# Optimization experiments

Measured on AMD Instinct MI355X. Metric: run time of the kernel, lower is better.

The kernel has to match this reference:

```python
import jax, jax.numpy as jnp
import numpy as np

IN_SIZE = 64
RES = 1024
B = 16
T = 2048
ALPHA = 0.5
SPECTRAL_RADIUS = 0.9


def setup_inputs() -> dict:
    key = jax.random.key(0)
    ks = jax.random.split(key, 8)
    # W_hh scaled so spectral radius ~ SPECTRAL_RADIUS (circular law: |eig|max ~ sqrt(R)*std)
    scale_hh = SPECTRAL_RADIUS / np.sqrt(RES)
    return {
        "x": jax.random.normal(ks[0], (B, T, IN_SIZE), dtype=jnp.float32),
        "W_in0": jax.random.normal(ks[1], (IN_SIZE, RES), dtype=jnp.float32) * 0.5,
        "W_hh0": jax.random.normal(ks[2], (RES, RES), dtype=jnp.float32) * scale_hh,
        "b0": jax.random.normal(ks[3], (1, RES), dtype=jnp.float32) * 0.5,
        "W_in1": jax.random.normal(ks[4], (RES, RES), dtype=jnp.float32) * 0.1,
        "W_hh1": jax.random.normal(ks[5], (RES, RES), dtype=jnp.float32) * scale_hh,
        "b1": jax.random.normal(ks[6], (1, RES), dtype=jnp.float32) * 0.5,
        "readout": jax.random.normal(ks[7], (2 * RES, IN_SIZE), dtype=jnp.float32) * 0.02,
    }


def _reservoir_layer(xs, W_in, W_hh, b, alpha):
    # xs: [T, B, F] time-major; sequential leaky-integrator scan over T
    h0 = jnp.zeros((xs.shape[1], W_hh.shape[0]), dtype=xs.dtype)

    def step(h, x_i):
        h = (1.0 - alpha) * h + alpha * jnp.tanh(x_i @ W_in + h @ W_hh + b)
        return h, h

    _, states = jax.lax.scan(step, h0, xs)
    return states  # [T, B, R]


def reference(x, W_in0, W_hh0, b0, W_in1, W_hh1, b1, readout):
    xt = jnp.transpose(x, (1, 0, 2))  # [T, B, in]
    s0 = _reservoir_layer(xt, W_in0, W_hh0, b0, ALPHA)  # [T, B, R]
    s1 = _reservoir_layer(s0, W_in1, W_hh1, b1, ALPHA)  # [T, B, R]
    h = jnp.concatenate([s0, s1], axis=-1)  # [T, B, 2R]
    out = h @ readout  # [T, B, in]
    return jnp.transpose(out, (1, 0, 2))  # [B, T, in]
```

## Files before the change

kernel.cpp:

```cpp
#include <hip/hip_runtime.h>
#include <math.h>

#define ESN_B 16
#define ESN_T 2048
#define ESN_R 1024
#define ESN_IN 64
#define NBR (ESN_B * ESN_R)

#define OFF_WT_HH0 0
#define OFF_WT_IN1 (1024 * 1024)
#define OFF_WT_HH1 (2 * 1024 * 1024)
#define OFF_WT_IN0 (3 * 1024 * 1024)
#define OFF_RT     (OFF_WT_IN0 + 1024 * 64)
#define OFF_S0G    (OFF_RT + 64 * 2048)
#define OFF_S1G    (OFF_S0G + 2 * NBR)
#define OFF_FLAGS  (OFF_S1G + 2 * NBR)

__global__ void __launch_bounds__(256) transpose_k(const float* __restrict__ src,
                                                   float* __restrict__ dst,
                                                   int rows, int cols) {
  __shared__ float tile[32][33];
  int bx = blockIdx.x * 32, by = blockIdx.y * 32;
  int tx = threadIdx.x, ty = threadIdx.y;
  #pragma unroll
  for (int i = ty; i < 32; i += 8) {
    int r = by + i, c = bx + tx;
    if (r < rows && c < cols) tile[i][tx] = src[(size_t)r * cols + c];
  }
  __syncthreads();
  #pragma unroll
  for (int i = ty; i < 32; i += 8) {
    int c = bx + i, r = by + tx;
    if (c < cols && r < rows) dst[(size_t)c * rows + r] = tile[tx][i];
  }
}

__device__ __forceinline__ float fast_tanh(float v) {
  float a = fabsf(v);
  float e = __expf(-2.0f * a);
  float t = __fdividef(1.0f - e, 1.0f + e);
  return copysignf(t, v);
}

__device__ __forceinline__ float dot4(float4 a, float4 b, float acc) {
  acc = fmaf(a.x, b.x, acc);
  acc = fmaf(a.y, b.y, acc);
  acc = fmaf(a.z, b.z, acc);
  acc = fmaf(a.w, b.w, acc);
  return acc;
}

__device__ __forceinline__ float wave_red64(float v) {
  #pragma unroll
  for (int off = 32; off > 0; off >>= 1) v += __shfl_xor(v, off, 64);
  return v;
}

__device__ __forceinline__ float reduce4(float a0, float a1, float a2, float a3,
                                         bool lb0, bool lb1) {
  float uA = lb0 ? a0 : a1, kA = lb0 ? a1 : a0;
  float A = kA + __shfl_xor(uA, 1, 64);
  float uB = lb0 ? a2 : a3, kB = lb0 ? a3 : a2;
  float B = kB + __shfl_xor(uB, 1, 64);
  float uC = lb1 ? A : B, kC = lb1 ? B : A;
  float C = kC + __shfl_xor(uC, 2, 64);
  C += __shfl_xor(C, 4, 64);
  C += __shfl_xor(C, 8, 64);
  C += __shfl_xor(C, 16, 64);
  C += __shfl_xor(C, 32, 64);
  return C;
}

__device__ __forceinline__ void llc_store_f32(float* p, float v) {
  asm volatile("global_store_dword %0, %1, off sc1" :: "v"(p), "v"(v) : "memory");
}
__device__ __forceinline__ void llc_store_u32(unsigned* p, unsigned v) {
  asm volatile("global_store_dword %0, %1, off sc1" :: "v"(p), "v"(v) : "memory");
}
__device__ __forceinline__ void vmcnt0() {
  asm volatile("s_waitcnt vmcnt(0)" ::: "memory");
}

__global__ void __launch_bounds__(256, 1) esn_scan_kernel(
    const float* __restrict__ x,
    const float* __restrict__ b0,
    const float* __restrict__ b1,
    float* __restrict__ wsf,
    float* __restrict__ out) {
  __shared__ float s0l[2][4][1024];
  __shared__ float s1l[4][1024];

  const float* wtHH0 = wsf + OFF_WT_HH0;
  const float* wtIN1 = wsf + OFF_WT_IN1;
  const float* wtHH1 = wsf + OFF_WT_HH1;
  const float* wtIN0 = wsf + OFF_WT_IN0;
  const float* rt    = wsf + OFF_RT;
  float* s0g = wsf + OFF_S0G;
  float* s1g = wsf + OFF_S1G;
  unsigned* flags = (unsigned*)(wsf + OFF_FLAGS);

  const int tid = threadIdx.x;
  const int l = tid & 63;
  const int w = tid >> 6;
  const int bid = blockIdx.x;
  const int g = bid >> 6;
  const int bg = bid & 63;
  const int batch0 = g * 4;
  const int c0 = (bg * 4 + w) * 4;
  const int wg = bg * 4 + w;
  const int rbl = wg >> 6;
  const int rb = batch0 + rbl;
  const int roc = wg & 63;
  unsigned* gflags = flags + g * 64;
  const bool lb0 = (l & 1) != 0;
  const bool lb1 = (l & 2) != 0;

  float4 whh0[4][4], win1[4][4], whh1[4][4], rdt[8];
  float win0v[4];
  #pragma unroll
  for (int cc = 0; cc < 4; ++cc) {
    const float* p0 = wtHH0 + (size_t)(c0 + cc) * ESN_R + l * 4;
    const float* p1 = wtIN1 + (size_t)(c0 + cc) * ESN_R + l * 4;
    const float* p2 = wtHH1 + (size_t)(c0 + cc) * ESN_R + l * 4;
    #pragma unroll
    for (int q = 0; q < 4; ++q) {
      whh0[cc][q] = *(const float4*)(p0 + q * 256);
      win1[cc][q] = *(const float4*)(p1 + q * 256);
      whh1[cc][q] = *(const float4*)(p2 + q * 256);
    }
    win0v[cc] = wtIN0[(size_t)(c0 + cc) * ESN_IN + l];
  }
  #pragma unroll
  for (int q = 0; q < 8; ++q)
    rdt[q] = *(const float4*)(rt + (size_t)roc * 2048 + q * 256 + l * 4);
  const float b0sel = b0[c0 + (l & 3)];
  const float b1sel = b1[c0 + (l & 3)];

  for (int r = 0; r < ESN_T + 2; ++r) {
    const int slot = r & 1, oslot = slot ^ 1;
    const bool doL0 = (r < ESN_T);
    const bool doL1 = (r >= 1 && r <= ESN_T);

    float xv[4];
    if (doL0) {
      #pragma unroll
      for (int bb = 0; bb < 4; ++bb)
        xv[bb] = x[((size_t)(batch0 + bb) * ESN_T + r) * ESN_IN + l];
    }

    if (r > 0) {
      if (w == 0) {
        const unsigned* fp = &gflags[l];
        unsigned f;
        do {
          asm volatile("global_load_dword %0, %1, off sc1\n\ts_waitcnt vmcnt(0)"
                       : "=v"(f) : "v"(fp) : "memory");
        } while (!__all(f >= (unsigned)r));
      }
      __syncthreads();
    }

    {
      const float* gs0 = s0g + oslot * NBR + batch0 * ESN_R + tid * 4;
      const float* gs1 = s1g + oslot * NBR + batch0 * ESN_R + tid * 4;
      float4 t0, t1, t2, t3, u0, u1, u2, u3;
      asm volatile(
          "global_load_dwordx4 %0, %8, off sc1\n\t"
          "global_load_dwordx4 %1, %9, off sc1\n\t"
          "global_load_dwordx4 %2, %10, off sc1\n\t"
          "global_load_dwordx4 %3, %11, off sc1\n\t"
          "global_load_dwordx4 %4, %12, off sc1\n\t"
          "global_load_dwordx4 %5, %13, off sc1\n\t"
          "global_load_dwordx4 %6, %14, off sc1\n\t"
          "global_load_dwordx4 %7, %15, off sc1\n\t"
          "s_waitcnt vmcnt(0)"
          : "=&v"(t0), "=&v"(t1), "=&v"(t2), "=&v"(t3),
            "=&v"(u0), "=&v"(u1), "=&v"(u2), "=&v"(u3)
          : "v"(gs0), "v"(gs0 + 1024), "v"(gs0 + 2048), "v"(gs0 + 3072),
            "v"(gs1), "v"(gs1 + 1024), "v"(gs1 + 2048), "v"(gs1 + 3072)
          : "memory");
      float* d0 = &s0l[slot][0][0] + tid * 4;
      float* d1 = &s1l[0][0] + tid * 4;
      *(float4*)(d0)        = t0;
      *(float4*)(d0 + 1024) = t1;
      *(float4*)(d0 + 2048) = t2;
      *(float4*)(d0 + 3072) = t3;
      *(float4*)(d1)        = u0;
      *(float4*)(d1 + 1024) = u1;
      *(float4*)(d1 + 2048) = u2;
      *(float4*)(d1 + 3072) = u3;
    }
    __syncthreads();

    for (int bb = 0; bb < 4; ++bb) {
      float4 h0f[4];
      #pragma unroll
      for (int q = 0; q < 4; ++q)
        h0f[q] = *(const float4*)(&s0l[slot][bb][q * 256 + l * 4]);

      if (doL0) {
        float a0 = xv[bb] * win0v[0], a1 = xv[bb] * win0v[1];
        float a2 = xv[bb] * win0v[2], a3 = xv[bb] * win0v[3];
        #pragma unroll
        for (int q = 0; q < 4; ++q) {
          a0 = dot4(whh0[0][q], h0f[q], a0);
          a1 = dot4(whh0[1][q], h0f[q], a1);
          a2 = dot4(whh0[2][q], h0f[q], a2);
          a3 = dot4(whh0[3][q], h0f[q], a3);
        }
        float C = reduce4(a0, a1, a2, a3, lb0, lb1);
        if (l < 4) {
          float prev = s0l[slot][bb][c0 + l];
          float nv = 0.5f * prev + 0.5f * fast_tanh(C + b0sel);
          llc_store_f32(&s0g[slot * NBR + (batch0 + bb) * ESN_R + c0 + l], nv);
        }
      }
      if (doL1) {
        float4 h1f[4];
        #pragma unroll
        for (int q = 0; q < 4; ++q)
          h1f[q] = *(const float4*)(&s1l[bb][q * 256 + l * 4]);
        float a0 = 0.f, a1 = 0.f, a2 = 0.f, a3 = 0.f;
        #pragma unroll
        for (int q = 0; q < 4; ++q) {
          a0 = dot4(win1[0][q], h0f[q], a0); a0 = dot4(whh1[0][q], h1f[q], a0);
          a1 = dot4(win1[1][q], h0f[q], a1); a1 = dot4(whh1[1][q], h1f[q], a1);
          a2 = dot4(win1[2][q], h0f[q], a2); a2 = dot4(whh1[2][q], h1f[q], a2);
          a3 = dot4(win1[3][q], h0f[q], a3); a3 = dot4(whh1[3][q], h1f[q], a3);
        }
        float C = reduce4(a0, a1, a2, a3, lb0, lb1);
        if (l < 4) {
          float prev = s1l[bb][c0 + l];
          float nv = 0.5f * prev + 0.5f * fast_tanh(C + b1sel);
          llc_store_f32(&s1g[slot * NBR + (batch0 + bb) * ESN_R + c0 + l], nv);
        }
      }
    }

    vmcnt0();
    __syncthreads();
    if (tid == 0) llc_store_u32(&gflags[bg], (unsigned)(r + 1));

    if (r >= 2) {
      float a = 0.f;
      #pragma unroll
      for (int q = 0; q < 4; ++q)
        a = dot4(rdt[q], *(const float4*)(&s0l[oslot][rbl][q * 256 + l * 4]), a);
      #pragma unroll
      for (int q = 0; q < 4; ++q)
        a = dot4(rdt[q + 4], *(const float4*)(&s1l[rbl][q * 256 + l * 4]), a);
      a = wave_red64(a);
      if (l == 0) out[((size_t)rb * ESN_T + (r - 2)) * ESN_IN + roc] = a;
    }
  }
}

extern "C" void kernel_launch(void* const* d_in, const int* in_sizes, int n_in,
                              void* d_out, int out_size, void* d_ws, size_t ws_size,
                              hipStream_t stream) {
  (void)in_sizes; (void)n_in; (void)out_size; (void)ws_size;
  const float* x     = (const float*)d_in[0];
  const float* w_in0 = (const float*)d_in[1];
  const float* w_hh0 = (const float*)d_in[2];
  const float* b0    = (const float*)d_in[3];
  const float* w_in1 = (const float*)d_in[4];
  const float* w_hh1 = (const float*)d_in[5];
  const float* b1    = (const float*)d_in[6];
  const float* rdo   = (const float*)d_in[7];
  float* out = (float*)d_out;
  float* wsf = (float*)d_ws;

  dim3 tb(32, 8);
  transpose_k<<<dim3(32, 32), tb, 0, stream>>>(w_hh0, wsf + OFF_WT_HH0, 1024, 1024);
  transpose_k<<<dim3(32, 32), tb, 0, stream>>>(w_in1, wsf + OFF_WT_IN1, 1024, 1024);
  transpose_k<<<dim3(32, 32), tb, 0, stream>>>(w_hh1, wsf + OFF_WT_HH1, 1024, 1024);
  transpose_k<<<dim3(32, 2),  tb, 0, stream>>>(w_in0, wsf + OFF_WT_IN0, 64, 1024);
  transpose_k<<<dim3(2, 64),  tb, 0, stream>>>(rdo,   wsf + OFF_RT, 2048, 64);

  hipMemsetAsync(wsf + OFF_S0G + NBR, 0, NBR * sizeof(float), stream);
  hipMemsetAsync(wsf + OFF_S1G, 0, NBR * sizeof(float), stream);
  hipMemsetAsync(wsf + OFF_FLAGS, 0, 4 * 64 * sizeof(unsigned), stream);

  esn_scan_kernel<<<dim3(256), dim3(256), 0, stream>>>(x, b0, b1, wsf, out);
}
```

Baseline: 13.83 ms.

## Split grid-wide step barrier into separate layer-0 and layer-1 flag phases

Replaces the single per-step cross-block flag barrier with two flag arrays, one per reservoir layer. Layer-0 state is staged, computed and published, and its flag is raised before layer-1 work begins. Layer 1 then waits on its own flag before staging and computing. The intent is to shorten the layer-0 recurrence critical path so other blocks can start the next step sooner. The cost is an extra global polling phase and more block-level synchronisation per timestep.

```diff
diff --git a/kernel.cpp b/kernel.cpp
--- a/kernel.cpp
+++ b/kernel.cpp
@@ -77,8 +77,33 @@
 __device__ __forceinline__ void llc_store_u32(unsigned* p, unsigned v) {
   asm volatile("global_store_dword %0, %1, off sc1" :: "v"(p), "v"(v) : "memory");
 }
+__device__ __forceinline__ unsigned llc_load_u32(const unsigned* p) {
+  unsigned f;
+  asm volatile("global_load_dword %0, %1, off sc1\n\ts_waitcnt vmcnt(0)"
+               : "=v"(f) : "v"(p) : "memory");
+  return f;
+}
 __device__ __forceinline__ void vmcnt0() {
   asm volatile("s_waitcnt vmcnt(0)" ::: "memory");
+}
+
+__device__ __forceinline__ void stage4k(const float* gsrc, float* ldst, int tid) {
+  float4 t0, t1, t2, t3;
+  const float* p = gsrc + tid * 4;
+  asm volatile(
+      "global_load_dwordx4 %0, %4, off sc1\n\t"
+      "global_load_dwordx4 %1, %5, off sc1\n\t"
+      "global_load_dwordx4 %2, %6, off sc1\n\t"
+      "global_load_dwordx4 %3, %7, off sc1\n\t"
+      "s_waitcnt vmcnt(0)"
+      : "=&v"(t0), "=&v"(t1), "=&v"(t2), "=&v"(t3)
+      : "v"(p), "v"(p + 1024), "v"(p + 2048), "v"(p + 3072)
+      : "memory");
+  float* d = ldst + tid * 4;
+  *(float4*)(d)        = t0;
+  *(float4*)(d + 1024) = t1;
+  *(float4*)(d + 2048) = t2;
+  *(float4*)(d + 3072) = t3;
 }
 
 __global__ void __launch_bounds__(256, 1) esn_scan_kernel(
@@ -111,7 +136,8 @@
   const int rbl = wg >> 6;
   const int rb = batch0 + rbl;
   const int roc = wg & 63;
-  unsigned* gflags = flags + g * 64;
+  unsigned* gflag0 = flags + g * 64;
+  unsigned* gflag1 = flags + 256 + g * 64;
   const bool lb0 = (l & 1) != 0;
   const bool lb1 = (l & 2) != 0;
 
@@ -150,55 +176,20 @@
 
     if (r > 0) {
       if (w == 0) {
-        const unsigned* fp = &gflags[l];
-        unsigned f;
-        do {
-          asm volatile("global_load_dword %0, %1, off sc1\n\ts_waitcnt vmcnt(0)"
-                       : "=v"(f) : "v"(fp) : "memory");
-        } while (!__all(f >= (unsigned)r));
+        while (!__all(llc_load_u32(&gflag0[l]) >= (unsigned)r)) {}
       }
       __syncthreads();
     }
 
-    {
-      const float* gs0 = s0g + oslot * NBR + batch0 * ESN_R + tid * 4;
-      const float* gs1 = s1g + oslot * NBR + batch0 * ESN_R + tid * 4;
-      float4 t0, t1, t2, t3, u0, u1, u2, u3;
-      asm volatile(
-          "global_load_dwordx4 %0, %8, off sc1\n\t"
-          "global_load_dwordx4 %1, %9, off sc1\n\t"
-          "global_load_dwordx4 %2, %10, off sc1\n\t"
-          "global_load_dwordx4 %3, %11, off sc1\n\t"
-          "global_load_dwordx4 %4, %12, off sc1\n\t"
-          "global_load_dwordx4 %5, %13, off sc1\n\t"
-          "global_load_dwordx4 %6, %14, off sc1\n\t"
-          "global_load_dwordx4 %7, %15, off sc1\n\t"
-          "s_waitcnt vmcnt(0)"
-          : "=&v"(t0), "=&v"(t1), "=&v"(t2), "=&v"(t3),
-            "=&v"(u0), "=&v"(u1), "=&v"(u2), "=&v"(u3)
-          : "v"(gs0), "v"(gs0 + 1024), "v"(gs0 + 2048), "v"(gs0 + 3072),
-            "v"(gs1), "v"(gs1 + 1024), "v"(gs1 + 2048), "v"(gs1 + 3072)
-          : "memory");
-      float* d0 = &s0l[slot][0][0] + tid * 4;
-      float* d1 = &s1l[0][0] + tid * 4;
-      *(float4*)(d0)        = t0;
-      *(float4*)(d0 + 1024) = t1;
-      *(float4*)(d0 + 2048) = t2;
-      *(float4*)(d0 + 3072) = t3;
-      *(float4*)(d1)        = u0;
-      *(float4*)(d1 + 1024) = u1;
-      *(float4*)(d1 + 2048) = u2;
-      *(float4*)(d1 + 3072) = u3;
-    }
-    __syncthreads();
-
-    for (int bb = 0; bb < 4; ++bb) {
-      float4 h0f[4];
-      #pragma unroll
-      for (int q = 0; q < 4; ++q)
-        h0f[q] = *(const float4*)(&s0l[slot][bb][q * 256 + l * 4]);
-
-      if (doL0) {
+    stage4k(s0g + oslot * NBR + batch0 * ESN_R, &s0l[slot][0][0], tid);
+    __syncthreads();
+
+    if (doL0) {
+      for (int bb = 0; bb < 4; ++bb) {
+        float4 h0f[4];
+        #pragma unroll
+        for (int q = 0; q < 4; ++q)
+          h0f[q] = *(const float4*)(&s0l[slot][bb][q * 256 + l * 4]);
         float a0 = xv[bb] * win0v[0], a1 = xv[bb] * win0v[1];
         float a2 = xv[bb] * win0v[2], a3 = xv[bb] * win0v[3];
         #pragma unroll
@@ -215,11 +206,29 @@
           llc_store_f32(&s0g[slot * NBR + (batch0 + bb) * ESN_R + c0 + l], nv);
         }
       }
-      if (doL1) {
-        float4 h1f[4];
-        #pragma unroll
-        for (int q = 0; q < 4; ++q)
+    }
+    vmcnt0();
+    __syncthreads();
+    if (tid == 0) llc_store_u32(&gflag0[bg], (unsigned)(r + 1));
+
+    if (r > 1) {
+      if (w == 0) {
+        while (!__all(llc_load_u32(&gflag1[l]) >= (unsigned)r)) {}
+      }
+    }
+    __syncthreads();
+
+    stage4k(s1g + oslot * NBR + batch0 * ESN_R, &s1l[0][0], tid);
+    __syncthreads();
+
+    if (doL1) {
+      for (int bb = 0; bb < 4; ++bb) {
+        float4 h0f[4], h1f[4];
+        #pragma unroll
+        for (int q = 0; q < 4; ++q) {
+          h0f[q] = *(const float4*)(&s0l[slot][bb][q * 256 + l * 4]);
           h1f[q] = *(const float4*)(&s1l[bb][q * 256 + l * 4]);
+        }
         float a0 = 0.f, a1 = 0.f, a2 = 0.f, a3 = 0.f;
         #pragma unroll
         for (int q = 0; q < 4; ++q) {
@@ -236,10 +245,9 @@
         }
       }
     }
-
     vmcnt0();
     __syncthreads();
-    if (tid == 0) llc_store_u32(&gflags[bg], (unsigned)(r + 1));
+    if (tid == 0) llc_store_u32(&gflag1[bg], (unsigned)(r + 1));
 
     if (r >= 2) {
       float a = 0.f;
@@ -279,7 +287,7 @@
 
   hipMemsetAsync(wsf + OFF_S0G + NBR, 0, NBR * sizeof(float), stream);
   hipMemsetAsync(wsf + OFF_S1G, 0, NBR * sizeof(float), stream);
-  hipMemsetAsync(wsf + OFF_FLAGS, 0, 4 * 64 * sizeof(unsigned), stream);
+  hipMemsetAsync(wsf + OFF_FLAGS, 0, 2 * 4 * 64 * sizeof(unsigned), stream);
 
   esn_scan_kernel<<<dim3(256), dim3(256), 0, stream>>>(x, b0, b1, wsf, out);
 }
```

After: 15.42 ms. 11.5% more time.
